# Kernel optimization log

Hardware: AMD Instinct MI355X
Metric: run time of the kernel (lower is better)

The kernel has to match this reference:

```python
import jax, jax.numpy as jnp
import numpy as np

C = 128
EPS = 1e-5

def _layernorm(x, w, b):
    mu = jnp.mean(x, axis=-1, keepdims=True)
    var = jnp.var(x, axis=-1, keepdims=True)
    return (x - mu) * jax.lax.rsqrt(var + EPS) * w + b

def setup_inputs() -> dict:
    key = jax.random.key(0)
    ks = jax.random.split(key, 8)
    B, N = 1, 512
    z = jax.random.normal(ks[0], (B, N, N, C), dtype=jnp.float32)
    pair_mask = jnp.ones((B, N, N), dtype=jnp.float32)
    s = 1.0 / np.sqrt(C)
    return {
        "z": z,
        "pair_mask": pair_mask,
        "ln_in_w": jnp.ones((C,), jnp.float32),
        "ln_in_b": jnp.zeros((C,), jnp.float32),
        "ln_out_w": jnp.ones((C,), jnp.float32),
        "ln_out_b": jnp.zeros((C,), jnp.float32),
        "w_pa": jax.random.normal(ks[1], (C, C), jnp.float32) * s,
        "w_pb": jax.random.normal(ks[2], (C, C), jnp.float32) * s,
        "w_ga": jax.random.normal(ks[3], (C, C), jnp.float32) * s,
        "w_gb": jax.random.normal(ks[4], (C, C), jnp.float32) * s,
        "w_g": jax.random.normal(ks[5], (C, C), jnp.float32) * s,
        "w_o": jax.random.normal(ks[6], (C, C), jnp.float32) * s,
    }

def reference(z, pair_mask, ln_in_w, ln_in_b, ln_out_w, ln_out_b,
              w_pa, w_pb, w_ga, w_gb, w_g, w_o):
    # z: (B,i,j,c), pair_mask: (B,i,j)
    zn = _layernorm(z, ln_in_w, ln_in_b)
    m = pair_mask[..., None]
    # gated, masked left/right projections (weights stored torch-style (out,in))
    a = m * jax.nn.sigmoid(zn @ w_ga.T) * (zn @ w_pa.T)  # (B,i,k,c)
    b = m * jax.nn.sigmoid(zn @ w_gb.T) * (zn @ w_pb.T)  # (B,j,k,c)
    # 'outgoing' triangular update: contract over shared k
    o = jnp.einsum('bikc,bjkc->bijc', a, b)
    on = _layernorm(o, ln_out_w, ln_out_b)
    g = jax.nn.sigmoid(zn @ w_g.T)
    return g * (on @ w_o.T)
```

## Files before the change

### kernel.cpp

```cpp
#include <hip/hip_runtime.h>
#include <hip/hip_fp16.h>


typedef unsigned short u16;
typedef unsigned int u32;
typedef unsigned short u16x8 __attribute__((ext_vector_type(8)));
typedef _Float16 f16;
typedef _Float16 f16x8 __attribute__((ext_vector_type(8)));
typedef _Float16 f16x2 __attribute__((ext_vector_type(2)));
typedef float f32x4 __attribute__((ext_vector_type(4)));

#define NROW 262144
#define CH 128

__device__ __forceinline__ float sigmoidf_(float x) {
  return 1.0f / (1.0f + __expf(-x));
}

__global__ __launch_bounds__(256) void k_pass0(
    const float* __restrict__ wpa, const float* __restrict__ wga,
    const float* __restrict__ wpb, const float* __restrict__ wgb,
    f16* __restrict__ wq) {
  const int m = blockIdx.x >> 6;
  const int idx = ((blockIdx.x & 63) << 8) + threadIdx.x;
  const float* src = (m == 0) ? wpa : (m == 1) ? wga : (m == 2) ? wpb : wgb;
  wq[(size_t)m * CH * CH + idx] = (f16)src[idx];
}

__global__ __launch_bounds__(256) void k_cvt2(
    const float* __restrict__ w_g, const float* __restrict__ w_o,
    f16* __restrict__ wq3) {
  const int m = blockIdx.x >> 6;
  const int idx = ((blockIdx.x & 63) << 8) + threadIdx.x;
  const float* src = (m == 0) ? w_g : w_o;
  wq3[(size_t)m * CH * CH + idx] = (f16)src[idx];
}

__global__ __launch_bounds__(256) void k_pass1(
    const float* __restrict__ z, const float* __restrict__ pm,
    const float* __restrict__ lnw, const float* __restrict__ lnb,
    const f16* __restrict__ wq,
    f16* __restrict__ a_t, f16* __restrict__ b_t) {
  __shared__ __attribute__((aligned(16))) f16 zn[64 * CH];
  __shared__ __attribute__((aligned(16))) f16 ab[CH * 64];
  __shared__ float pmv[64];
  const int t = threadIdx.x, lane = t & 63, w = t >> 6;
  const size_t r0 = (size_t)blockIdx.x * 64;

  {
    const int rr = lane >> 4, q = lane & 15;
    const float4 lw0 = *(const float4*)(lnw + q * 8);
    const float4 lw1 = *(const float4*)(lnw + q * 8 + 4);
    const float4 lb0 = *(const float4*)(lnb + q * 8);
    const float4 lb1 = *(const float4*)(lnb + q * 8 + 4);
    for (int it = 0; it < 4; it++) {
      const int row = w * 16 + it * 4 + rr;
      const float* src = z + (r0 + row) * CH + q * 8;
      const float4 v0 = *(const float4*)(src);
      const float4 v1 = *(const float4*)(src + 4);
      float s = v0.x + v0.y + v0.z + v0.w + v1.x + v1.y + v1.z + v1.w;
      float sq = v0.x * v0.x + v0.y * v0.y + v0.z * v0.z + v0.w * v0.w +
                 v1.x * v1.x + v1.y * v1.y + v1.z * v1.z + v1.w * v1.w;
#pragma unroll
      for (int off = 8; off > 0; off >>= 1) {
        s += __shfl_xor(s, off);
        sq += __shfl_xor(sq, off);
      }
      const float mu = s * (1.0f / 128.0f);
      const float rs = rsqrtf(sq * (1.0f / 128.0f) - mu * mu + 1e-5f);
      f16x8 p;
      p[0] = (f16)((v0.x - mu) * rs * lw0.x + lb0.x);
      p[1] = (f16)((v0.y - mu) * rs * lw0.y + lb0.y);
      p[2] = (f16)((v0.z - mu) * rs * lw0.z + lb0.z);
      p[3] = (f16)((v0.w - mu) * rs * lw0.w + lb0.w);
      p[4] = (f16)((v1.x - mu) * rs * lw1.x + lb1.x);
      p[5] = (f16)((v1.y - mu) * rs * lw1.y + lb1.y);
      p[6] = (f16)((v1.z - mu) * rs * lw1.z + lb1.z);
      p[7] = (f16)((v1.w - mu) * rs * lw1.w + lb1.w);
      const int byte = (row * 256 + q * 16) ^ ((row & 7) << 4);
      *(f16x8*)((char*)zn + byte) = p;
      if (q == 0) pmv[row] = pm[r0 + row];
    }
  }
  __syncthreads();

  const int g = lane >> 4, ln16 = lane & 15;
#pragma unroll
  for (int pair = 0; pair < 2; pair++) {
    const f16* __restrict__ wp = wq + (size_t)(pair * 2 + 0) * CH * CH;
    const f16* __restrict__ wgp = wq + (size_t)(pair * 2 + 1) * CH * CH;
#pragma unroll
    for (int f = 0; f < 2; f++) {
      const int col = w * 32 + f * 16 + ln16;
      f16x8 bp[4], bg[4];
#pragma unroll
      for (int ks = 0; ks < 4; ks++) {
        const size_t wo = (size_t)col * CH + ks * 32 + g * 8;
        bp[ks] = *(const f16x8*)(wp + wo);
        bg[ks] = *(const f16x8*)(wgp + wo);
      }
#pragma unroll
      for (int mt = 0; mt < 4; mt++) {
        const int m0 = mt * 16;
        const int row = m0 + ln16;
        f32x4 accP = {0.f, 0.f, 0.f, 0.f}, accG = {0.f, 0.f, 0.f, 0.f};
#pragma unroll
        for (int ks = 0; ks < 4; ks++) {
          const int byte =
              (row * 256 + (ks * 32 + g * 8) * 2) ^ ((row & 7) << 4);
          const f16x8 af = *(const f16x8*)((const char*)zn + byte);
          accP = __builtin_amdgcn_mfma_f32_16x16x32_f16(af, bp[ks], accP, 0, 0, 0);
          accG = __builtin_amdgcn_mfma_f32_16x16x32_f16(af, bg[ks], accG, 0, 0, 0);
        }
        uint2 pk;
        {
          const int rbase = m0 + g * 4;
          const float v0 = pmv[rbase + 0] * sigmoidf_(accG[0]) * accP[0];
          const float v1 = pmv[rbase + 1] * sigmoidf_(accG[1]) * accP[1];
          const float v2 = pmv[rbase + 2] * sigmoidf_(accG[2]) * accP[2];
          const float v3 = pmv[rbase + 3] * sigmoidf_(accG[3]) * accP[3];
          f16x2 h01, h23;
          h01.x = (f16)v0; h01.y = (f16)v1;
          h23.x = (f16)v2; h23.y = (f16)v3;
          pk.x = *(u32*)&h01;
          pk.y = *(u32*)&h23;
        }
        const int byte = ((col * 64 + m0 + g * 4) * 2) ^ ((col & 7) << 4);
        *(uint2*)((char*)ab + byte) = pk;
      }
    }
    __syncthreads();
    {
      const int o = t >> 1, h = t & 1;
      f16* __restrict__ dst =
          (pair ? b_t : a_t) + (size_t)o * NROW + r0 + h * 32;
#pragma unroll
      for (int e = 0; e < 4; e++) {
        const int byte = ((o * 64 + h * 32 + e * 8) * 2) ^ ((o & 7) << 4);
        *(uint4*)(dst + e * 8) = *(const uint4*)((const char*)ab + byte);
      }
    }
    if (pair == 0) __syncthreads();
  }
}

__global__ __launch_bounds__(256, 4) void k_pass2(
    const f16* __restrict__ a_t, const f16* __restrict__ b_t,
    f16* __restrict__ o16) {
  __shared__ __attribute__((aligned(16))) f16 smem[2 * 128 * 64];
  f16* At = smem;
  f16* Bt = smem + 128 * 64;
  const int t = threadIdx.x, lane = t & 63, w = t >> 6;
  const int bx = blockIdx.x;
  const int xcd = bx & 7, k = bx >> 3;
  const int T = k & 15, cc = k >> 4;
  const int c = xcd + (cc << 3);
  const int i0 = (T >> 2) * 128, j0 = (T & 3) * 128;
  const int wr = w >> 1, wc = w & 1;
  const int g = lane >> 4, ln16 = lane & 15;

  const f16* __restrict__ Ab = a_t + (size_t)c * NROW + (size_t)i0 * 512;
  const f16* __restrict__ Bb = b_t + (size_t)c * NROW + (size_t)j0 * 512;

  const int srow = t >> 1, shalf = t & 1;
  const f16* __restrict__ gA = Ab + (size_t)srow * 512 + shalf * 32;
  const f16* __restrict__ gB = Bb + (size_t)srow * 512 + shalf * 32;
  int swb[4];
#pragma unroll
  for (int q = 0; q < 4; q++)
    swb[q] = srow * 128 + ((shalf * 64 + q * 16) ^ ((srow & 7) << 4));

  f32x4 acc[4][4];
#pragma unroll
  for (int mt = 0; mt < 4; mt++)
#pragma unroll
    for (int nt = 0; nt < 4; nt++) acc[mt][nt] = {0.f, 0.f, 0.f, 0.f};

  uint4 va[4], vb[4];
#pragma unroll
  for (int q = 0; q < 4; q++) {
    va[q] = *(const uint4*)(gA + q * 8);
    vb[q] = *(const uint4*)(gB + q * 8);
  }
#pragma unroll
  for (int q = 0; q < 4; q++) {
    *(uint4*)((char*)At + swb[q]) = va[q];
    *(uint4*)((char*)Bt + swb[q]) = vb[q];
  }
  __syncthreads();

  for (int ks = 0; ks < 8; ks++) {
    const bool more = (ks + 1) < 8;
    if (more) {
#pragma unroll
      for (int q = 0; q < 4; q++) {
        va[q] = *(const uint4*)(gA + (ks + 1) * 64 + q * 8);
        vb[q] = *(const uint4*)(gB + (ks + 1) * 64 + q * 8);
      }
    }
    f16x8 bfr[4][2];
#pragma unroll
    for (int nt = 0; nt < 4; nt++)
#pragma unroll
      for (int kk = 0; kk < 2; kk++) {
        const int row = wc * 64 + nt * 16 + ln16;
        const int byte = row * 128 + ((kk * 64 + g * 16) ^ ((row & 7) << 4));
        bfr[nt][kk] = *(const f16x8*)((const char*)Bt + byte);
      }
#pragma unroll
    for (int mt = 0; mt < 4; mt++) {
      f16x8 afr[2];
#pragma unroll
      for (int kk = 0; kk < 2; kk++) {
        const int row = wr * 64 + mt * 16 + ln16;
        const int byte = row * 128 + ((kk * 64 + g * 16) ^ ((row & 7) << 4));
        afr[kk] = *(const f16x8*)((const char*)At + byte);
      }
#pragma unroll
      for (int nt = 0; nt < 4; nt++) {
        acc[mt][nt] =
            __builtin_amdgcn_mfma_f32_16x16x32_f16(afr[0], bfr[nt][0], acc[mt][nt], 0, 0, 0);
        acc[mt][nt] =
            __builtin_amdgcn_mfma_f32_16x16x32_f16(afr[1], bfr[nt][1], acc[mt][nt], 0, 0, 0);
      }
    }
    __syncthreads();
    if (more) {
#pragma unroll
      for (int q = 0; q < 4; q++) {
        *(uint4*)((char*)At + swb[q]) = va[q];
        *(uint4*)((char*)Bt + swb[q]) = vb[q];
      }
      __syncthreads();
    }
  }

  f16* otile = smem;
#pragma unroll
  for (int mt = 0; mt < 4; mt++)
#pragma unroll
    for (int reg = 0; reg < 4; reg++) {
      const int il = wr * 64 + mt * 16 + g * 4 + reg;
#pragma unroll
      for (int nt = 0; nt < 4; nt++) {
        const int jl = wc * 64 + nt * 16 + ln16;
        const int byte = (il * 256 + jl * 2) ^ ((il & 7) << 4);
        *(f16*)((char*)otile + byte) = (f16)acc[mt][nt][reg];
      }
    }
  __syncthreads();
  {
    const int i = t >> 1, jh = t & 1;
    f16* __restrict__ dst =
        o16 + (size_t)c * NROW + (size_t)(i0 + i) * 512 + j0 + jh * 64;
#pragma unroll
    for (int e = 0; e < 8; e++) {
      const int byte = (i * 256 + jh * 128 + e * 16) ^ ((i & 7) << 4);
      *(uint4*)(dst + e * 8) = *(const uint4*)((const char*)otile + byte);
    }
  }
}

__global__ __launch_bounds__(256) void k_pass3a(
    const f16* __restrict__ o16,
    const float* __restrict__ lnwo, const float* __restrict__ lnbo,
    f16* __restrict__ on_t) {
  __shared__ __attribute__((aligned(16))) f16 ot[64 * CH];
  const int t = threadIdx.x, lane = t & 63, w = t >> 6;
  const size_t r0 = (size_t)blockIdx.x * 64;

  {
    const int c = t >> 1, rh = t & 1;
    const f16* src = o16 + (size_t)c * NROW + r0 + rh * 32;
    u16x8 d[4];
#pragma unroll
    for (int q = 0; q < 4; q++) d[q] = *(const u16x8*)((const u16*)src + q * 8);
#pragma unroll
    for (int i = 0; i < 32; i++) {
      const int r = rh * 32 + i;
      const int byte = (r * 256 + c * 2) ^ ((r & 7) << 4);
      *(u16*)((char*)ot + byte) = d[i >> 3][i & 7];
    }
  }
  __syncthreads();

  {
    const int rr = lane >> 4, q = lane & 15;
    const float4 lw0 = *(const float4*)(lnwo + q * 8);
    const float4 lw1 = *(const float4*)(lnwo + q * 8 + 4);
    const float4 lb0 = *(const float4*)(lnbo + q * 8);
    const float4 lb1 = *(const float4*)(lnbo + q * 8 + 4);
    for (int it = 0; it < 4; it++) {
      const int row = w * 16 + it * 4 + rr;
      const int byte = (row * 256 + q * 16) ^ ((row & 7) << 4);
      const f16x8 v = *(const f16x8*)((const char*)ot + byte);
      float x[8];
#pragma unroll
      for (int e = 0; e < 8; e++) x[e] = (float)v[e];
      float s = 0.f, sq = 0.f;
#pragma unroll
      for (int e = 0; e < 8; e++) { s += x[e]; sq += x[e] * x[e]; }
#pragma unroll
      for (int off = 8; off > 0; off >>= 1) {
        s += __shfl_xor(s, off);
        sq += __shfl_xor(sq, off);
      }
      const float mu = s * (1.0f / 128.0f);
      const float rs = rsqrtf(sq * (1.0f / 128.0f) - mu * mu + 1e-5f);
      f16x8 p;
      p[0] = (f16)((x[0] - mu) * rs * lw0.x + lb0.x);
      p[1] = (f16)((x[1] - mu) * rs * lw0.y + lb0.y);
      p[2] = (f16)((x[2] - mu) * rs * lw0.z + lb0.z);
      p[3] = (f16)((x[3] - mu) * rs * lw0.w + lb0.w);
      p[4] = (f16)((x[4] - mu) * rs * lw1.x + lb1.x);
      p[5] = (f16)((x[5] - mu) * rs * lw1.y + lb1.y);
      p[6] = (f16)((x[6] - mu) * rs * lw1.z + lb1.z);
      p[7] = (f16)((x[7] - mu) * rs * lw1.w + lb1.w);
      *(f16x8*)(on_t + (r0 + row) * CH + q * 8) = p;
    }
  }
}

__global__ __launch_bounds__(256) void k_pass3b(
    const float* __restrict__ z,
    const float* __restrict__ lnwi, const float* __restrict__ lnbi,
    const f16* __restrict__ on_t,
    const f16* __restrict__ wq3,
    float* __restrict__ out) {
  __shared__ __attribute__((aligned(16))) f16 zn[64 * CH];
  __shared__ __attribute__((aligned(16))) f16 on[64 * CH];
  const int t = threadIdx.x, lane = t & 63, w = t >> 6;
  const size_t r0 = (size_t)blockIdx.x * 64;

  {
    const int row = t >> 2, ch0 = (t & 3) * 32;
    const u16* src = (const u16*)(on_t + (r0 + row) * CH + ch0);
#pragma unroll
    for (int e = 0; e < 4; e++) {
      const uint4 v = *(const uint4*)(src + e * 8);
      const int byte = (row * 256 + (ch0 + e * 8) * 2) ^ ((row & 7) << 4);
      *(uint4*)((char*)on + byte) = v;
    }
  }
  {
    const int rr = lane >> 4, q = lane & 15;
    const float4 lw0 = *(const float4*)(lnwi + q * 8);
    const float4 lw1 = *(const float4*)(lnwi + q * 8 + 4);
    const float4 lb0 = *(const float4*)(lnbi + q * 8);
    const float4 lb1 = *(const float4*)(lnbi + q * 8 + 4);
    for (int it = 0; it < 4; it++) {
      const int row = w * 16 + it * 4 + rr;
      const float* src = z + (r0 + row) * CH + q * 8;
      const float4 v0 = *(const float4*)(src);
      const float4 v1 = *(const float4*)(src + 4);
      float s = v0.x + v0.y + v0.z + v0.w + v1.x + v1.y + v1.z + v1.w;
      float sq = v0.x * v0.x + v0.y * v0.y + v0.z * v0.z + v0.w * v0.w +
                 v1.x * v1.x + v1.y * v1.y + v1.z * v1.z + v1.w * v1.w;
#pragma unroll
      for (int off = 8; off > 0; off >>= 1) {
        s += __shfl_xor(s, off);
        sq += __shfl_xor(sq, off);
      }
      const float mu = s * (1.0f / 128.0f);
      const float rs = rsqrtf(sq * (1.0f / 128.0f) - mu * mu + 1e-5f);
      f16x8 p;
      p[0] = (f16)((v0.x - mu) * rs * lw0.x + lb0.x);
      p[1] = (f16)((v0.y - mu) * rs * lw0.y + lb0.y);
      p[2] = (f16)((v0.z - mu) * rs * lw0.z + lb0.z);
      p[3] = (f16)((v0.w - mu) * rs * lw0.w + lb0.w);
      p[4] = (f16)((v1.x - mu) * rs * lw1.x + lb1.x);
      p[5] = (f16)((v1.y - mu) * rs * lw1.y + lb1.y);
      p[6] = (f16)((v1.z - mu) * rs * lw1.z + lb1.z);
      p[7] = (f16)((v1.w - mu) * rs * lw1.w + lb1.w);
      const int byte = (row * 256 + q * 16) ^ ((row & 7) << 4);
      *(f16x8*)((char*)zn + byte) = p;
    }
  }
  __syncthreads();

  const int g = lane >> 4, ln16 = lane & 15;
  const f16* __restrict__ wg = wq3;
  const f16* __restrict__ wo = wq3 + (size_t)CH * CH;
#pragma unroll
  for (int f = 0; f < 2; f++) {
    const int col = w * 32 + f * 16 + ln16;
    f16x8 bg[4], bo[4];
#pragma unroll
    for (int ks = 0; ks < 4; ks++) {
      const size_t woff = (size_t)col * CH + ks * 32 + g * 8;
      bg[ks] = *(const f16x8*)(wg + woff);
      bo[ks] = *(const f16x8*)(wo + woff);
    }
#pragma unroll
    for (int mt = 0; mt < 4; mt++) {
      const int m0 = mt * 16;
      const int row = m0 + ln16;
      f32x4 accG = {0.f, 0.f, 0.f, 0.f}, accP = {0.f, 0.f, 0.f, 0.f};
#pragma unroll
      for (int ks = 0; ks < 4; ks++) {
        const int byte =
            (row * 256 + (ks * 32 + g * 8) * 2) ^ ((row & 7) << 4);
        const f16x8 az = *(const f16x8*)((const char*)zn + byte);
        const f16x8 ao = *(const f16x8*)((const char*)on + byte);
        accG = __builtin_amdgcn_mfma_f32_16x16x32_f16(az, bg[ks], accG, 0, 0, 0);
        accP = __builtin_amdgcn_mfma_f32_16x16x32_f16(ao, bo[ks], accP, 0, 0, 0);
      }
#pragma unroll
      for (int reg = 0; reg < 4; reg++) {
        const int orow = m0 + g * 4 + reg;
        out[(r0 + orow) * CH + col] = sigmoidf_(accG[reg]) * accP[reg];
      }
    }
  }
}

extern "C" void kernel_launch(void* const* d_in, const int* in_sizes, int n_in,
                              void* d_out, int out_size, void* d_ws, size_t ws_size,
                              hipStream_t stream) {
  const float* z = (const float*)d_in[0];
  const float* pm = (const float*)d_in[1];
  const float* ln_in_w = (const float*)d_in[2];
  const float* ln_in_b = (const float*)d_in[3];
  const float* ln_out_w = (const float*)d_in[4];
  const float* ln_out_b = (const float*)d_in[5];
  const float* w_pa = (const float*)d_in[6];
  const float* w_pb = (const float*)d_in[7];
  const float* w_ga = (const float*)d_in[8];
  const float* w_gb = (const float*)d_in[9];
  const float* w_g = (const float*)d_in[10];
  const float* w_o = (const float*)d_in[11];

  f16* a_t = (f16*)d_ws;
  f16* b_t = a_t + (size_t)CH * NROW;
  float* out = (float*)d_out;
  f16* wq = (f16*)d_out;
  f16* o16 = (f16*)d_out;
  f16* wq3 = (f16*)d_ws;
  f16* on_t = b_t;

  k_pass0<<<256, 256, 0, stream>>>(w_pa, w_ga, w_pb, w_gb, wq);
  k_pass1<<<4096, 256, 0, stream>>>(z, pm, ln_in_w, ln_in_b, wq, a_t, b_t);
  k_pass2<<<2048, 256, 0, stream>>>(a_t, b_t, o16);
  k_cvt2<<<128, 256, 0, stream>>>(w_g, w_o, wq3);
  k_pass3a<<<4096, 256, 0, stream>>>(o16, ln_out_w, ln_out_b, on_t);
  k_pass3b<<<4096, 256, 0, stream>>>(z, ln_in_w, ln_in_b, on_t, wq3, out);
}
```

Before: 652.8 us.

## Restructure triangle GEMM to full-row tiles writing in place, fuse out-LN into final pass

The per-channel GEMM now gives each block all 512 rows of A against a 128-column slice of B. Each block writes its result straight into the B buffer, in a per-slice layout. This is safe only because the block reading that B slice is the same block that later overwrites it, after all its loads are done. The separate output-LayerNorm pass is folded into the final gating and projection kernel, which removes one full fp16 round trip of the intermediate tensor and one launch. The cost is 512-thread blocks at one block per CU with a larger accumulator, fewer blocks (512), and more K steps with smaller K chunks.

```diff
diff --git a/kernel.cpp b/kernel.cpp
--- a/kernel.cpp
+++ b/kernel.cpp
@@ -144,202 +144,129 @@
   }
 }
 
-__global__ __launch_bounds__(256, 4) void k_pass2(
-    const f16* __restrict__ a_t, const f16* __restrict__ b_t,
-    f16* __restrict__ o16) {
-  __shared__ __attribute__((aligned(16))) f16 smem[2 * 128 * 64];
-  f16* At = smem;
-  f16* Bt = smem + 128 * 64;
+__global__ __launch_bounds__(512, 1) void k_pass2(
+    const f16* __restrict__ a_t, f16* bt) {
+  __shared__ __attribute__((aligned(16))) f16 At[512 * 32];
+  __shared__ __attribute__((aligned(16))) f16 Bt[128 * 32];
   const int t = threadIdx.x, lane = t & 63, w = t >> 6;
   const int bx = blockIdx.x;
-  const int xcd = bx & 7, k = bx >> 3;
-  const int T = k & 15, cc = k >> 4;
-  const int c = xcd + (cc << 3);
-  const int i0 = (T >> 2) * 128, j0 = (T & 3) * 128;
-  const int wr = w >> 1, wc = w & 1;
+  const int xcd = bx & 7, s = bx >> 3;
+  const int c = xcd + ((s >> 2) << 3);
+  const int js = s & 3;
   const int g = lane >> 4, ln16 = lane & 15;
 
-  const f16* __restrict__ Ab = a_t + (size_t)c * NROW + (size_t)i0 * 512;
-  const f16* __restrict__ Bb = b_t + (size_t)c * NROW + (size_t)j0 * 512;
-
-  const int srow = t >> 1, shalf = t & 1;
-  const f16* __restrict__ gA = Ab + (size_t)srow * 512 + shalf * 32;
-  const f16* __restrict__ gB = Bb + (size_t)srow * 512 + shalf * 32;
-  int swb[4];
+  const f16* gA = a_t + (size_t)c * NROW + (size_t)t * 512;
+  const f16* gB = bt + (size_t)c * NROW +
+                  (size_t)(js * 128 + (t >> 2)) * 512 + (t & 3) * 8;
+  const int aRow = t, bRow = t >> 2, bChunk = t & 3;
+
+  f32x4 acc[4][8];
+#pragma unroll
+  for (int mt = 0; mt < 4; mt++)
+#pragma unroll
+    for (int nt = 0; nt < 8; nt++) acc[mt][nt] = {0.f, 0.f, 0.f, 0.f};
+
+  uint4 va[4];
+  uint4 vb;
+#pragma unroll
+  for (int q = 0; q < 4; q++) va[q] = *(const uint4*)(gA + q * 8);
+  vb = *(const uint4*)(gB);
 #pragma unroll
   for (int q = 0; q < 4; q++)
-    swb[q] = srow * 128 + ((shalf * 64 + q * 16) ^ ((srow & 7) << 4));
-
-  f32x4 acc[4][4];
-#pragma unroll
-  for (int mt = 0; mt < 4; mt++)
-#pragma unroll
-    for (int nt = 0; nt < 4; nt++) acc[mt][nt] = {0.f, 0.f, 0.f, 0.f};
-
-  uint4 va[4], vb[4];
-#pragma unroll
-  for (int q = 0; q < 4; q++) {
-    va[q] = *(const uint4*)(gA + q * 8);
-    vb[q] = *(const uint4*)(gB + q * 8);
-  }
-#pragma unroll
-  for (int q = 0; q < 4; q++) {
-    *(uint4*)((char*)At + swb[q]) = va[q];
-    *(uint4*)((char*)Bt + swb[q]) = vb[q];
-  }
+    *(uint4*)((char*)At + aRow * 64 + ((q * 16) ^ ((aRow & 3) << 4))) = va[q];
+  *(uint4*)((char*)Bt + bRow * 64 + ((bChunk * 16) ^ ((bRow & 3) << 4))) = vb;
   __syncthreads();
 
-  for (int ks = 0; ks < 8; ks++) {
-    const bool more = (ks + 1) < 8;
+  for (int ks = 0; ks < 16; ks++) {
+    const bool more = (ks + 1) < 16;
     if (more) {
 #pragma unroll
-      for (int q = 0; q < 4; q++) {
-        va[q] = *(const uint4*)(gA + (ks + 1) * 64 + q * 8);
-        vb[q] = *(const uint4*)(gB + (ks + 1) * 64 + q * 8);
-      }
-    }
-    f16x8 bfr[4][2];
-#pragma unroll
-    for (int nt = 0; nt < 4; nt++)
-#pragma unroll
-      for (int kk = 0; kk < 2; kk++) {
-        const int row = wc * 64 + nt * 16 + ln16;
-        const int byte = row * 128 + ((kk * 64 + g * 16) ^ ((row & 7) << 4));
-        bfr[nt][kk] = *(const f16x8*)((const char*)Bt + byte);
-      }
+      for (int q = 0; q < 4; q++)
+        va[q] = *(const uint4*)(gA + (ks + 1) * 32 + q * 8);
+      vb = *(const uint4*)(gB + (ks + 1) * 32);
+    }
+    f16x8 bfr[8];
+#pragma unroll
+    for (int nt = 0; nt < 8; nt++) {
+      const int row = nt * 16 + ln16;
+      bfr[nt] = *(const f16x8*)((const char*)Bt + row * 64 +
+                                ((g * 16) ^ ((row & 3) << 4)));
+    }
 #pragma unroll
     for (int mt = 0; mt < 4; mt++) {
-      f16x8 afr[2];
-#pragma unroll
-      for (int kk = 0; kk < 2; kk++) {
-        const int row = wr * 64 + mt * 16 + ln16;
-        const int byte = row * 128 + ((kk * 64 + g * 16) ^ ((row & 7) << 4));
-        afr[kk] = *(const f16x8*)((const char*)At + byte);
-      }
-#pragma unroll
-      for (int nt = 0; nt < 4; nt++) {
+      const int row = w * 64 + mt * 16 + ln16;
+      const f16x8 afr = *(const f16x8*)((const char*)At + row * 64 +
+                                        ((g * 16) ^ ((row & 3) << 4)));
+#pragma unroll
+      for (int nt = 0; nt < 8; nt++)
         acc[mt][nt] =
-            __builtin_amdgcn_mfma_f32_16x16x32_f16(afr[0], bfr[nt][0], acc[mt][nt], 0, 0, 0);
-        acc[mt][nt] =
-            __builtin_amdgcn_mfma_f32_16x16x32_f16(afr[1], bfr[nt][1], acc[mt][nt], 0, 0, 0);
-      }
+            __builtin_amdgcn_mfma_f32_16x16x32_f16(afr, bfr[nt], acc[mt][nt], 0, 0, 0);
     }
     __syncthreads();
     if (more) {
 #pragma unroll
-      for (int q = 0; q < 4; q++) {
-        *(uint4*)((char*)At + swb[q]) = va[q];
-        *(uint4*)((char*)Bt + swb[q]) = vb[q];
-      }
+      for (int q = 0; q < 4; q++)
+        *(uint4*)((char*)At + aRow * 64 + ((q * 16) ^ ((aRow & 3) << 4))) = va[q];
+      *(uint4*)((char*)Bt + bRow * 64 + ((bChunk * 16) ^ ((bRow & 3) << 4))) = vb;
       __syncthreads();
     }
   }
-
-  f16* otile = smem;
-#pragma unroll
-  for (int mt = 0; mt < 4; mt++)
-#pragma unroll
-    for (int reg = 0; reg < 4; reg++) {
-      const int il = wr * 64 + mt * 16 + g * 4 + reg;
-#pragma unroll
-      for (int nt = 0; nt < 4; nt++) {
-        const int jl = wc * 64 + nt * 16 + ln16;
-        const int byte = (il * 256 + jl * 2) ^ ((il & 7) << 4);
-        *(f16*)((char*)otile + byte) = (f16)acc[mt][nt][reg];
-      }
-    }
   __syncthreads();
-  {
-    const int i = t >> 1, jh = t & 1;
-    f16* __restrict__ dst =
-        o16 + (size_t)c * NROW + (size_t)(i0 + i) * 512 + j0 + jh * 64;
-#pragma unroll
-    for (int e = 0; e < 8; e++) {
-      const int byte = (i * 256 + jh * 128 + e * 16) ^ ((i & 7) << 4);
-      *(uint4*)(dst + e * 8) = *(const uint4*)((const char*)otile + byte);
-    }
-  }
-}
-
-__global__ __launch_bounds__(256) void k_pass3a(
-    const f16* __restrict__ o16,
-    const float* __restrict__ lnwo, const float* __restrict__ lnbo,
-    f16* __restrict__ on_t) {
-  __shared__ __attribute__((aligned(16))) f16 ot[64 * CH];
-  const int t = threadIdx.x, lane = t & 63, w = t >> 6;
-  const size_t r0 = (size_t)blockIdx.x * 64;
-
-  {
-    const int c = t >> 1, rh = t & 1;
-    const f16* src = o16 + (size_t)c * NROW + r0 + rh * 32;
-    u16x8 d[4];
-#pragma unroll
-    for (int q = 0; q < 4; q++) d[q] = *(const u16x8*)((const u16*)src + q * 8);
-#pragma unroll
-    for (int i = 0; i < 32; i++) {
-      const int r = rh * 32 + i;
-      const int byte = (r * 256 + c * 2) ^ ((r & 7) << 4);
-      *(u16*)((char*)ot + byte) = d[i >> 3][i & 7];
-    }
-  }
-  __syncthreads();
-
-  {
-    const int rr = lane >> 4, q = lane & 15;
-    const float4 lw0 = *(const float4*)(lnwo + q * 8);
-    const float4 lw1 = *(const float4*)(lnwo + q * 8 + 4);
-    const float4 lb0 = *(const float4*)(lnbo + q * 8);
-    const float4 lb1 = *(const float4*)(lnbo + q * 8 + 4);
-    for (int it = 0; it < 4; it++) {
-      const int row = w * 16 + it * 4 + rr;
-      const int byte = (row * 256 + q * 16) ^ ((row & 7) << 4);
-      const f16x8 v = *(const f16x8*)((const char*)ot + byte);
-      float x[8];
-#pragma unroll
-      for (int e = 0; e < 8; e++) x[e] = (float)v[e];
-      float s = 0.f, sq = 0.f;
-#pragma unroll
-      for (int e = 0; e < 8; e++) { s += x[e]; sq += x[e] * x[e]; }
-#pragma unroll
-      for (int off = 8; off > 0; off >>= 1) {
-        s += __shfl_xor(s, off);
-        sq += __shfl_xor(sq, off);
-      }
-      const float mu = s * (1.0f / 128.0f);
-      const float rs = rsqrtf(sq * (1.0f / 128.0f) - mu * mu + 1e-5f);
-      f16x8 p;
-      p[0] = (f16)((x[0] - mu) * rs * lw0.x + lb0.x);
-      p[1] = (f16)((x[1] - mu) * rs * lw0.y + lb0.y);
-      p[2] = (f16)((x[2] - mu) * rs * lw0.z + lb0.z);
-      p[3] = (f16)((x[3] - mu) * rs * lw0.w + lb0.w);
-      p[4] = (f16)((x[4] - mu) * rs * lw1.x + lb1.x);
-      p[5] = (f16)((x[5] - mu) * rs * lw1.y + lb1.y);
-      p[6] = (f16)((x[6] - mu) * rs * lw1.z + lb1.z);
-      p[7] = (f16)((x[7] - mu) * rs * lw1.w + lb1.w);
-      *(f16x8*)(on_t + (r0 + row) * CH + q * 8) = p;
-    }
-  }
-}
-
-__global__ __launch_bounds__(256) void k_pass3b(
+
+  char* lbase = (char*)At + w * 4096;
+  f16* dstBase = bt + (size_t)c * NROW + (size_t)js * 65536;
+#pragma unroll
+  for (int mt = 0; mt < 4; mt++) {
+#pragma unroll
+    for (int nt = 0; nt < 8; nt++)
+#pragma unroll
+      for (int reg = 0; reg < 4; reg++) {
+        const int il = g * 4 + reg;
+        const int jj = nt * 16 + ln16;
+        const int byte = (il * 256 + jj * 2) ^ ((il & 7) << 4);
+        *(f16*)(lbase + byte) = (f16)acc[mt][nt][reg];
+      }
+    __syncthreads();
+    {
+      const int il2 = lane >> 2, ch = lane & 3;
+      f16* dst = dstBase + (size_t)(w * 64 + mt * 16 + il2) * 128 + ch * 32;
+#pragma unroll
+      for (int e = 0; e < 4; e++) {
+        const int byte = (il2 * 256 + ch * 64 + e * 16) ^ ((il2 & 7) << 4);
+        *(uint4*)(dst + e * 8) = *(const uint4*)(lbase + byte);
+      }
+    }
+    __syncthreads();
+  }
+}
+
+__global__ __launch_bounds__(256) void k_pass3(
     const float* __restrict__ z,
     const float* __restrict__ lnwi, const float* __restrict__ lnbi,
-    const f16* __restrict__ on_t,
+    const float* __restrict__ lnwo, const float* __restrict__ lnbo,
+    const f16* __restrict__ o16s,
     const f16* __restrict__ wq3,
     float* __restrict__ out) {
   __shared__ __attribute__((aligned(16))) f16 zn[64 * CH];
   __shared__ __attribute__((aligned(16))) f16 on[64 * CH];
   const int t = threadIdx.x, lane = t & 63, w = t >> 6;
   const size_t r0 = (size_t)blockIdx.x * 64;
+  const int i = (int)(r0 >> 9);
+  const int j0 = (int)(r0 & 511);
+  const int js = j0 >> 7, jl0 = j0 & 127;
 
   {
-    const int row = t >> 2, ch0 = (t & 3) * 32;
-    const u16* src = (const u16*)(on_t + (r0 + row) * CH + ch0);
-#pragma unroll
-    for (int e = 0; e < 4; e++) {
-      const uint4 v = *(const uint4*)(src + e * 8);
-      const int byte = (row * 256 + (ch0 + e * 8) * 2) ^ ((row & 7) << 4);
-      *(uint4*)((char*)on + byte) = v;
+    const int c = t >> 1, h = t & 1;
+    const f16* src = o16s + (size_t)c * NROW + (size_t)js * 65536 +
+                     (size_t)i * 128 + jl0 + h * 32;
+    u16x8 d[4];
+#pragma unroll
+    for (int q = 0; q < 4; q++) d[q] = *(const u16x8*)((const u16*)src + q * 8);
+#pragma unroll
+    for (int idx = 0; idx < 32; idx++) {
+      const int rloc = h * 32 + idx;
+      const int byte = (rloc * 256 + c * 2) ^ ((rloc & 7) << 4);
+      *(u16*)((char*)on + byte) = d[idx >> 3][idx & 7];
     }
   }
   {
@@ -374,6 +301,43 @@
       p[7] = (f16)((v1.w - mu) * rs * lw1.w + lb1.w);
       const int byte = (row * 256 + q * 16) ^ ((row & 7) << 4);
       *(f16x8*)((char*)zn + byte) = p;
+    }
+  }
+  __syncthreads();
+
+  {
+    const int rr = lane >> 4, q = lane & 15;
+    const float4 lw0 = *(const float4*)(lnwo + q * 8);
+    const float4 lw1 = *(const float4*)(lnwo + q * 8 + 4);
+    const float4 lb0 = *(const float4*)(lnbo + q * 8);
+    const float4 lb1 = *(const float4*)(lnbo + q * 8 + 4);
+    for (int it = 0; it < 4; it++) {
+      const int row = w * 16 + it * 4 + rr;
+      const int byte = (row * 256 + q * 16) ^ ((row & 7) << 4);
+      const f16x8 v = *(const f16x8*)((const char*)on + byte);
+      float x[8];
+#pragma unroll
+      for (int e = 0; e < 8; e++) x[e] = (float)v[e];
+      float s = 0.f, sq = 0.f;
+#pragma unroll
+      for (int e = 0; e < 8; e++) { s += x[e]; sq += x[e] * x[e]; }
+#pragma unroll
+      for (int off = 8; off > 0; off >>= 1) {
+        s += __shfl_xor(s, off);
+        sq += __shfl_xor(sq, off);
+      }
+      const float mu = s * (1.0f / 128.0f);
+      const float rs = rsqrtf(sq * (1.0f / 128.0f) - mu * mu + 1e-5f);
+      f16x8 p;
+      p[0] = (f16)((x[0] - mu) * rs * lw0.x + lb0.x);
+      p[1] = (f16)((x[1] - mu) * rs * lw0.y + lb0.y);
+      p[2] = (f16)((x[2] - mu) * rs * lw0.z + lb0.z);
+      p[3] = (f16)((x[3] - mu) * rs * lw0.w + lb0.w);
+      p[4] = (f16)((x[4] - mu) * rs * lw1.x + lb1.x);
+      p[5] = (f16)((x[5] - mu) * rs * lw1.y + lb1.y);
+      p[6] = (f16)((x[6] - mu) * rs * lw1.z + lb1.z);
+      p[7] = (f16)((x[7] - mu) * rs * lw1.w + lb1.w);
+      *(f16x8*)((char*)on + byte) = p;
     }
   }
   __syncthreads();
@@ -434,14 +398,12 @@
   f16* b_t = a_t + (size_t)CH * NROW;
   float* out = (float*)d_out;
   f16* wq = (f16*)d_out;
-  f16* o16 = (f16*)d_out;
   f16* wq3 = (f16*)d_ws;
-  f16* on_t = b_t;
 
   k_pass0<<<256, 256, 0, stream>>>(w_pa, w_ga, w_pb, w_gb, wq);
   k_pass1<<<4096, 256, 0, stream>>>(z, pm, ln_in_w, ln_in_b, wq, a_t, b_t);
-  k_pass2<<<2048, 256, 0, stream>>>(a_t, b_t, o16);
+  k_pass2<<<512, 512, 0, stream>>>(a_t, b_t);
   k_cvt2<<<128, 256, 0, stream>>>(w_g, w_o, wq3);
-  k_pass3a<<<4096, 256, 0, stream>>>(o16, ln_out_w, ln_out_b, on_t);
-  k_pass3b<<<4096, 256, 0, stream>>>(z, ln_in_w, ln_in_b, on_t, wq3, out);
-}
+  k_pass3<<<4096, 256, 0, stream>>>(z, ln_in_w, ln_in_b, ln_out_w, ln_out_b,
+                                    b_t, wq3, out);
+}
```

Measured after the change: 534.4 us. -18.1%, faster.
